# Kernel optimization log

Measured on AMD Instinct MI355X. Metric: run time of the kernel, lower is better.

## Reference

```python
import jax, jax.numpy as jnp
import numpy as np

B, J, HID, INTER, NL = 4096, 16, 128, 64, 4
NEG = -9.0e15
EDGES = [(0,1),(1,2),(2,3),(0,4),(4,5),(5,6),(0,7),(7,8),(8,9),(8,10),(10,11),(11,12),(8,13),(13,14),(14,15)]
GROUPED = [0,7,1,4,2,5,3,6,8,10,9,13,11,14,12,15]  # flattened nodes_group


def _adjacency_nonzeros():
    A = np.zeros((J, J), np.float32)
    for i, j in EDGES:
        A[i, j] = 1.0
        A[j, i] = 1.0
    A += np.eye(J, dtype=np.float32)
    rows, cols = np.nonzero(A)  # row-major, matches torch adj[mask] = e fill order
    return rows.astype(np.int32), cols.astype(np.int32)


def setup_inputs() -> dict:
    key = jax.random.key(0)
    ks = iter(jax.random.split(key, 64))
    rn = lambda shape, s: jax.random.normal(next(ks), shape, jnp.float32) * s
    rows, cols = _adjacency_nonzeros()
    nnz = rows.shape[0]  # 46
    inp = dict(
        x=jax.random.normal(next(ks), (B, J, 2), jnp.float32),
        # input SemGraphConv (2 -> HID) + its BatchNorm
        gc_in_W=rn((2, 2, HID), 0.7), gc_in_e=1.0 + rn((nnz,), 0.3), gc_in_b=rn((HID,), 0.05),
        bn_in_g=1.0 + rn((HID,), 0.05), bn_in_b=rn((HID,), 0.05),
        # 4 residual blocks x 2 graph convs (HID -> HID)
        W_res=rn((2 * NL, 2, HID, HID), 0.08), e_res=1.0 + rn((2 * NL, nnz), 0.3),
        b_res=rn((2 * NL, HID), 0.05),
        bng_res=1.0 + rn((2 * NL, HID), 0.05), bnb_res=rn((2 * NL, HID), 0.05),
        # 5 GraphNonLocal blocks (1 after input + 1 per residual block)
        nl_g_w=rn((NL + 1, INTER, HID), 0.08), nl_g_b=rn((NL + 1, INTER), 0.05),
        nl_t_w=rn((NL + 1, INTER, HID), 0.08), nl_t_b=rn((NL + 1, INTER), 0.05),
        nl_p_w=rn((NL + 1, INTER, HID), 0.08), nl_p_b=rn((NL + 1, INTER), 0.05),
        nl_cp_w=rn((NL + 1, 2 * INTER), 0.08),  # concat_project 1x1 conv, no bias
        nl_W_w=rn((NL + 1, HID, INTER), 0.08), nl_W_b=rn((NL + 1, HID), 0.05),
        nl_bn_g=1.0 + rn((NL + 1, HID), 0.05), nl_bn_b=rn((NL + 1, HID), 0.05),
        # output SemGraphConv (HID -> 3)
        gc_out_W=rn((2, HID, 3), 0.08), gc_out_e=1.0 + rn((nnz,), 0.3), gc_out_b=rn((3,), 0.05),
        # integer constants
        mask_rows=jnp.asarray(rows), mask_cols=jnp.asarray(cols),
        grouped_order=jnp.asarray(GROUPED, jnp.int32),
        restored_order=jnp.asarray(np.argsort(GROUPED), jnp.int32),
    )
    return inp


def reference(x, gc_in_W, gc_in_e, gc_in_b, bn_in_g, bn_in_b,
              W_res, e_res, b_res, bng_res, bnb_res,
              nl_g_w, nl_g_b, nl_t_w, nl_t_b, nl_p_w, nl_p_b,
              nl_cp_w, nl_W_w, nl_W_b, nl_bn_g, nl_bn_b,
              gc_out_W, gc_out_e, gc_out_b,
              mask_rows, mask_cols, grouped_order, restored_order):
    eye = jnp.eye(J, dtype=x.dtype)

    def gconv(h, W, e, b):
        # h: [B, J, F]
        h0 = jnp.einsum('bjf,fo->bjo', h, W[0])
        h1 = jnp.einsum('bjf,fo->bjo', h, W[1])
        logits = jnp.full((J, J), NEG, h.dtype).at[mask_rows, mask_cols].set(e)
        adj = jax.nn.softmax(logits, axis=1)
        diag = jnp.diagonal(adj)                     # adj*I picks diagonal scaling
        off = adj * (1.0 - eye)
        return diag[None, :, None] * h0 + jnp.einsum('ij,bjo->bio', off, h1) + b

    def bn(h, g, bta, axes):
        # training-mode BatchNorm (biased variance), per-channel
        m = h.mean(axes, keepdims=True)
        v = h.var(axes, keepdims=True)
        return (h - m) * jax.lax.rsqrt(v + 1e-5) * g + bta

    def graph_conv(h, W, e, b, gm, gb):
        h = gconv(h, W, e, b)
        h = bn(h, gm[None, None, :], gb[None, None, :], (0, 1))
        return jax.nn.relu(h)

    def nonlocal_block(h, i):
        xo = h[:, grouped_order]          # [B, J, C] regroup joints
        xc = xo.transpose(0, 2, 1)        # [B, C, J]
        conv = lambda w, bb: jnp.einsum('oc,bcj->boj', w, xc) + bb[None, :, None]
        pool = lambda t: t.reshape(B, INTER, J // 2, 2).max(-1)   # MaxPool1d(k=2)
        gx = pool(conv(nl_g_w[i], nl_g_b[i]))                     # [B, I, J/2]
        th = conv(nl_t_w[i], nl_t_b[i])                           # [B, I, J]
        ph = pool(conv(nl_p_w[i], nl_p_b[i]))                     # [B, I, J/2]
        wt, wp = nl_cp_w[i][:INTER], nl_cp_w[i][INTER:]
        # concat_project 1x1 conv over concat(theta,phi) decomposes into a sum
        f = jax.nn.relu(jnp.einsum('bch,c->bh', th, wt)[:, :, None]
                        + jnp.einsum('bcw,c->bw', ph, wp)[:, None, :])  # [B, J, J/2]
        f = f / (J // 2)
        y = jnp.einsum('bhw,bcw->bch', f, gx)                     # [B, I, J]
        Wy = jnp.einsum('oc,bch->boh', nl_W_w[i], y) + nl_W_b[i][None, :, None]
        Wy = bn(Wy, nl_bn_g[i][None, :, None], nl_bn_b[i][None, :, None], (0, 2))
        z = Wy + xc
        return z.transpose(0, 2, 1)[:, restored_order]

    out = graph_conv(x, gc_in_W, gc_in_e, gc_in_b, bn_in_g, bn_in_b)
    out = nonlocal_block(out, 0)
    for i in range(NL):
        res = out
        out = graph_conv(out, W_res[2 * i], e_res[2 * i], b_res[2 * i], bng_res[2 * i], bnb_res[2 * i])
        out = graph_conv(out, W_res[2 * i + 1], e_res[2 * i + 1], b_res[2 * i + 1], bng_res[2 * i + 1], bnb_res[2 * i + 1])
        out = res + out
        out = nonlocal_block(out, i + 1)
    return gconv(out, gc_out_W, gc_out_e, gc_out_b)  # [B, J, 3]
```

## Files before the change

kernel.cpp:

```cpp
#include <hip/hip_runtime.h>

#define B 4096
#define J 16
#define HID 128
#define INTER 64
#define NLAYERS 4
#define NEGV -9000000000000000.0f
#define ELEMS ((size_t)B*16*128)
#define NREP 16
#define SLOT 4096

typedef __attribute__((ext_vector_type(8))) short short8;
typedef __attribute__((ext_vector_type(4))) float f32x4;

static __device__ __forceinline__ unsigned short f2bf(float x) {
    unsigned u = __float_as_uint(x);
    unsigned r = u + 0x7fffu + ((u >> 16) & 1u);
    return (unsigned short)(r >> 16);
}
static __device__ __forceinline__ void splitbf(float x, unsigned short& h, unsigned short& l) {
    h = f2bf(x);
    float hf = __uint_as_float((unsigned)h << 16);
    l = f2bf(x - hf);
}
static __device__ __forceinline__ void splitbf4(float4 v, uint2& hh, uint2& ll) {
    unsigned short h0,l0,h1,l1,h2,l2,h3,l3;
    splitbf(v.x,h0,l0); splitbf(v.y,h1,l1); splitbf(v.z,h2,l2); splitbf(v.w,h3,l3);
    hh = make_uint2((unsigned)h0 | ((unsigned)h1<<16), (unsigned)h2 | ((unsigned)h3<<16));
    ll = make_uint2((unsigned)l0 | ((unsigned)l1<<16), (unsigned)l2 | ((unsigned)l3<<16));
}
static __device__ __forceinline__ f32x4 mfma16(short8 a, short8 b, f32x4 c) {
    return __builtin_amdgcn_mfma_f32_16x16x32_bf16(a, b, c, 0, 0, 0);
}
static __device__ __forceinline__ f32x4 mfma_split(short8 ah, short8 al,
                                                   short8 bh, short8 bl, f32x4 acc) {
    acc = mfma16(ah, bh, acc);
    acc = mfma16(ah, bl, acc);
    acc = mfma16(al, bh, acc);
    return acc;
}
static __device__ __forceinline__ float bfpair(unsigned short h, unsigned short l) {
    return __uint_as_float((unsigned)h << 16) + __uint_as_float((unsigned)l << 16);
}

__global__ void adj_kernel(const float* __restrict__ e_in,
                           const float* __restrict__ e_res,
                           const float* __restrict__ e_out,
                           const int* __restrict__ rows,
                           const int* __restrict__ cols, int nnz,
                           float* __restrict__ off_all,
                           float* __restrict__ diag_all) {
    int m = blockIdx.x;
    int i = threadIdx.x;
    const float* e = (m == 0) ? e_in : (m <= 8) ? e_res + (size_t)(m - 1) * nnz : e_out;
    float l[16];
    for (int j = 0; j < 16; j++) l[j] = NEGV;
    for (int k = 0; k < nnz; k++)
        if (rows[k] == i) l[cols[k]] = e[k];
    float mx = l[0];
    for (int j = 1; j < 16; j++) mx = fmaxf(mx, l[j]);
    float ex[16], s = 0.f;
    for (int j = 0; j < 16; j++) { ex[j] = expf(l[j] - mx); s += ex[j]; }
    float inv = 1.f / s;
    for (int j = 0; j < 16; j++) {
        float a = ex[j] * inv;
        if (j == i) { diag_all[m * 16 + i] = a; a = 0.f; }
        off_all[m * 256 + i * 16 + j] = a;
    }
}

#define WB_N   262144
#define NLW_N  122880
#define NLWW_N 40960
__global__ void prep_w_kernel(const float* __restrict__ W_res,
                              const float* __restrict__ g_w, const float* __restrict__ t_w,
                              const float* __restrict__ p_w, const float* __restrict__ W_w,
                              unsigned short* __restrict__ Wbh, unsigned short* __restrict__ Wbl,
                              unsigned short* __restrict__ nlwh, unsigned short* __restrict__ nlwl,
                              unsigned short* __restrict__ nlWh, unsigned short* __restrict__ nlWl) {
    int i = blockIdx.x * 256 + threadIdx.x;
    unsigned short h, l;
    if (i < WB_N) {
        int lay = i >> 15, rem = i & 32767, n = rem >> 8, k = rem & 255;
        int d = k >> 7, f = k & 127;
        splitbf(W_res[(((lay << 1) | d) * 128 + f) * 128 + n], h, l);
        Wbh[i] = h; Wbl[i] = l;
    } else if (i < WB_N + NLW_N) {
        int j = i - WB_N;
        int lay = j / 24576, r2 = j % 24576;
        int conv = r2 >> 13, oc = r2 & 8191;
        const float* src = conv == 0 ? g_w : conv == 1 ? t_w : p_w;
        splitbf(src[lay * 8192 + oc], h, l);
        nlwh[j] = h; nlwl[j] = l;
    } else if (i < WB_N + NLW_N + NLWW_N) {
        int j = i - WB_N - NLW_N;
        splitbf(W_w[j], h, l);
        nlWh[j] = h; nlWl[j] = l;
    }
}

__global__ void prep_vt_kernel(const float* __restrict__ t_w, const float* __restrict__ t_b,
                               const float* __restrict__ cp_w,
                               float* __restrict__ vt, float* __restrict__ ct) {
    int l = blockIdx.x, c = threadIdx.x;
    float s = 0.f;
    for (int c2 = 0; c2 < 64; c2++)
        s += cp_w[l * 128 + c2] * t_w[(l * 64 + c2) * 128 + c];
    vt[l * 128 + c] = s;
    if (c == 0) {
        float s2 = 0.f;
        for (int c2 = 0; c2 < 64; c2++) s2 += cp_w[l * 128 + c2] * t_b[l * 64 + c2];
        ct[l] = s2;
    }
}

__global__ void finalize_kernel(const float* __restrict__ slot, float* __restrict__ fin) {
    __shared__ float sh[256];
    int t = threadIdx.x;
    float s = 0.f;
    #pragma unroll
    for (int r = 0; r < NREP; r++) s += slot[r * 256 + t];
    sh[t] = s;
    __syncthreads();
    if (t < 128) {
        float m = sh[t] * (1.f / 65536.f);
        float v = sh[128 + t] * (1.f / 65536.f) - m * m;
        fin[t] = m;
        fin[128 + t] = rsqrtf(v + 1e-5f);
    }
}

__global__ __launch_bounds__(256) void gconv_in_kernel(
        const float* __restrict__ x, const float* __restrict__ W,
        const float* __restrict__ bias, const float* __restrict__ off,
        const float* __restrict__ diag, float* __restrict__ out,
        float* __restrict__ stats_out) {
    __shared__ float xs[16][2];
    __shared__ float gs[16][2];
    __shared__ float red[512];
    int b = blockIdx.x, t = threadIdx.x;
    if (t < 32) xs[t >> 1][t & 1] = x[b * 32 + t];
    __syncthreads();
    if (t < 32) {
        int i = t >> 1, f = t & 1;
        float g = 0.f;
        #pragma unroll
        for (int j = 0; j < 16; j++) g += off[i * 16 + j] * xs[j][f];
        gs[i][f] = g;
    }
    __syncthreads();
    int o = t & 127;
    float w00 = W[o], w01 = W[128 + o], w10 = W[256 + o], w11 = W[384 + o], bo = bias[o];
    float s = 0.f, q = 0.f;
    for (int idx = t; idx < 2048; idx += 256) {
        int i = idx >> 7;
        float v = diag[i] * (xs[i][0] * w00 + xs[i][1] * w01)
                + gs[i][0] * w10 + gs[i][1] * w11 + bo;
        out[(size_t)b * 2048 + idx] = v;
        s += v; q += v * v;
    }
    red[t] = s; red[256 + t] = q;
    __syncthreads();
    float* so = stats_out + (b & (NREP - 1)) * 256;
    if (t < 128) {
        atomicAdd(&so[t], red[t] + red[t + 128]);
        atomicAdd(&so[128 + t], red[256 + t] + red[256 + t + 128]);
    }
}

__global__ __launch_bounds__(256) void gconv_mfma_kernel(
        const float* src, const float* wy,
        const float* __restrict__ fin,
        const float* __restrict__ bn_g, const float* __restrict__ bn_b,
        const int* __restrict__ restored, float* zdst,
        const unsigned short* __restrict__ Wbh,
        const unsigned short* __restrict__ Wbl,
        const float* __restrict__ bias,
        const float* __restrict__ off, const float* __restrict__ diag,
        float* dst, float* __restrict__ stats_out) {
    __shared__ float hraw[16][132];
    __shared__ __align__(16) unsigned short ksh[16][264];
    __shared__ __align__(16) unsigned short ksl[16][264];
    __shared__ float offs[256];
    __shared__ float diags[16];
    int t = threadIdx.x;
    offs[t] = off[t];
    if (t < 16) diags[t] = diag[t];
    int c4 = (4 * t) & 127;
    int r0 = t >> 5;
    float4 m4 = make_float4(0,0,0,0), sc4 = make_float4(0,0,0,0), bb4 = make_float4(0,0,0,0);
    if (fin) {
        m4 = *(const float4*)&fin[c4];
        float4 iv = *(const float4*)&fin[128 + c4];
        float4 g4 = *(const float4*)&bn_g[c4];
        bb4 = *(const float4*)&bn_b[c4];
        sc4 = make_float4(iv.x * g4.x, iv.y * g4.y, iv.z * g4.z, iv.w * g4.w);
    }
    int ro0 = 0, ro1 = 0;
    if (wy) { ro0 = restored[r0]; ro1 = restored[r0 + 8]; }
    int b0 = blockIdx.x;
    const float4* src4 = (const float4*)src;
    const float4* wy4  = (const float4*)wy;
    float4 sv0 = src4[(size_t)b0 * 512 + t];
    float4 sv1 = src4[(size_t)b0 * 512 + 256 + t];
    float4 wv0 = make_float4(0,0,0,0), wv1 = make_float4(0,0,0,0);
    if (wy) {
        wv0 = wy4[(size_t)b0 * 512 + ro0 * 32 + (c4 >> 2)];
        wv1 = wy4[(size_t)b0 * 512 + ro1 * 32 + (c4 >> 2)];
    }
    int wv_ = t >> 6, lane = t & 63;
    int mn = lane & 15, kq = (lane >> 4) << 3, qr = (lane >> 4) << 2;

    for (int s = 0; s < 2; s++) {
        int bb_ = blockIdx.x + s * 2048;
        {
            float4 v = sv0;
            if (wy) {
                v.x += (wv0.x - m4.x) * sc4.x + bb4.x;
                v.y += (wv0.y - m4.y) * sc4.y + bb4.y;
                v.z += (wv0.z - m4.z) * sc4.z + bb4.z;
                v.w += (wv0.w - m4.w) * sc4.w + bb4.w;
                ((float4*)zdst)[(size_t)bb_ * 512 + t] = v;
            } else if (fin) {
                v.x = fmaxf((v.x - m4.x) * sc4.x + bb4.x, 0.f);
                v.y = fmaxf((v.y - m4.y) * sc4.y + bb4.y, 0.f);
                v.z = fmaxf((v.z - m4.z) * sc4.z + bb4.z, 0.f);
                v.w = fmaxf((v.w - m4.w) * sc4.w + bb4.w, 0.f);
            }
            *(float4*)&hraw[r0][c4] = v;
            v = sv1;
            if (wy) {
                v.x += (wv1.x - m4.x) * sc4.x + bb4.x;
                v.y += (wv1.y - m4.y) * sc4.y + bb4.y;
                v.z += (wv1.z - m4.z) * sc4.z + bb4.z;
                v.w += (wv1.w - m4.w) * sc4.w + bb4.w;
                ((float4*)zdst)[(size_t)bb_ * 512 + 256 + t] = v;
            } else if (fin) {
                v.x = fmaxf((v.x - m4.x) * sc4.x + bb4.x, 0.f);
                v.y = fmaxf((v.y - m4.y) * sc4.y + bb4.y, 0.f);
                v.z = fmaxf((v.z - m4.z) * sc4.z + bb4.z, 0.f);
                v.w = fmaxf((v.w - m4.w) * sc4.w + bb4.w, 0.f);
            }
            *(float4*)&hraw[r0 + 8][c4] = v;
        }
        if (s == 0) {
            int b1 = blockIdx.x + 2048;
            sv0 = src4[(size_t)b1 * 512 + t];
            sv1 = src4[(size_t)b1 * 512 + 256 + t];
            if (wy) {
                wv0 = wy4[(size_t)b1 * 512 + ro0 * 32 + (c4 >> 2)];
                wv1 = wy4[(size_t)b1 * 512 + ro1 * 32 + (c4 >> 2)];
            }
        }
        __syncthreads();
        for (int u = t; u < 512; u += 256) {
            int i = u >> 5, f4 = (u & 31) << 2;
            float4 hv = *(const float4*)&hraw[i][f4];
            float4 g = make_float4(0.f, 0.f, 0.f, 0.f);
            #pragma unroll
            for (int j = 0; j < 16; j++) {
                float w = offs[i * 16 + j];
                float4 hj = *(const float4*)&hraw[j][f4];
                g.x += w * hj.x; g.y += w * hj.y; g.z += w * hj.z; g.w += w * hj.w;
            }
            float d = diags[i];
            uint2 hh, ll;
            splitbf4(make_float4(d * hv.x, d * hv.y, d * hv.z, d * hv.w), hh, ll);
            *(uint2*)&ksh[i][f4] = hh;
            *(uint2*)&ksl[i][f4] = ll;
            splitbf4(g, hh, ll);
            *(uint2*)&ksh[i][128 + f4] = hh;
            *(uint2*)&ksl[i][128 + f4] = ll;
        }
        __syncthreads();
        int n0 = wv_ << 5;
        f32x4 acc0 = {0.f, 0.f, 0.f, 0.f}, acc1 = {0.f, 0.f, 0.f, 0.f};
        const unsigned short* wh0 = Wbh + (size_t)(n0 + mn) * 256 + kq;
        const unsigned short* wl0 = Wbl + (size_t)(n0 + mn) * 256 + kq;
        #pragma unroll
        for (int k = 0; k < 8; k++) {
            int k0 = k << 5;
            short8 ah = *(const short8*)&ksh[mn][k0 + kq];
            short8 al = *(const short8*)&ksl[mn][k0 + kq];
            acc0 = mfma_split(ah, al, *(const short8*)(wh0 + k0), *(const short8*)(wl0 + k0), acc0);
            acc1 = mfma_split(ah, al, *(const short8*)(wh0 + 4096 + k0), *(const short8*)(wl0 + 4096 + k0), acc1);
        }
        float bias0 = bias[n0 + mn], bias1 = bias[n0 + 16 + mn];
        float s0 = 0.f, q0 = 0.f, s1 = 0.f, q1 = 0.f;
        #pragma unroll
        for (int r = 0; r < 4; r++) {
            int row = qr + r;
            float v0 = acc0[r] + bias0;
            float v1 = acc1[r] + bias1;
            dst[(size_t)bb_ * 2048 + row * 128 + n0 + mn] = v0;
            dst[(size_t)bb_ * 2048 + row * 128 + n0 + 16 + mn] = v1;
            s0 += v0; q0 += v0 * v0; s1 += v1; q1 += v1 * v1;
        }
        s0 += __shfl_xor(s0, 16); s0 += __shfl_xor(s0, 32);
        q0 += __shfl_xor(q0, 16); q0 += __shfl_xor(q0, 32);
        s1 += __shfl_xor(s1, 16); s1 += __shfl_xor(s1, 32);
        q1 += __shfl_xor(q1, 16); q1 += __shfl_xor(q1, 32);
        float* so = stats_out + (bb_ & (NREP - 1)) * 256;
        if (lane < 16) {
            atomicAdd(&so[n0 + mn], s0);
            atomicAdd(&so[128 + n0 + mn], q0);
            atomicAdd(&so[n0 + 16 + mn], s1);
            atomicAdd(&so[128 + n0 + 16 + mn], q1);
        }
        if (s == 0) __syncthreads();
    }
}

#define CG(conv, o, j) cgbuf[((conv) * 64 + (o)) * 17 + (j)]
#define WYL(o, j)      cgbuf[(o) * 17 + (j)]
__global__ __launch_bounds__(512) void nl_a_kernel(
        const float* tsrc, const float* __restrict__ fin,
        const float* __restrict__ bn_g, const float* __restrict__ bn_b,
        const float* res,
        const unsigned short* __restrict__ nlwh,
        const unsigned short* __restrict__ nlwl,
        const float* __restrict__ g_b, const float* __restrict__ p_b,
        const float* __restrict__ cpw,
        const float* __restrict__ vt, const float* __restrict__ ctp,
        const unsigned short* __restrict__ nlWh,
        const unsigned short* __restrict__ nlWl,
        const float* __restrict__ W_b,
        const int* __restrict__ restored,
        float* hdst, float* wydst, float* __restrict__ wst) {
    __shared__ __align__(16) unsigned short xch[16][136];
    __shared__ __align__(16) unsigned short xcl[16][136];
    __shared__ float cgbuf[2176];
    __shared__ float gx[64][9];
    __shared__ float tvp[16][4], pvp[8][8];
    __shared__ float tv[16], pv[8];
    __shared__ float vtl[128];
    __shared__ __align__(16) unsigned short ybh[16][72];
    __shared__ __align__(16) unsigned short ybl[16][72];
    __shared__ float redS[512], redQ[512];
    int b = blockIdx.x, t = threadIdx.x;
    {
        if (t < 128) vtl[t] = vt[t];
        int c4 = (4 * t) & 127;
        int r = t >> 5;
        float4 m4 = *(const float4*)&fin[c4];
        float4 iv = *(const float4*)&fin[128 + c4];
        float4 g4 = *(const float4*)&bn_g[c4];
        float4 bb4 = *(const float4*)&bn_b[c4];
        float4 sc4 = make_float4(iv.x * g4.x, iv.y * g4.y, iv.z * g4.z, iv.w * g4.w);
        float4 v = ((const float4*)tsrc)[(size_t)b * 512 + t];
        v.x = fmaxf((v.x - m4.x) * sc4.x + bb4.x, 0.f);
        v.y = fmaxf((v.y - m4.y) * sc4.y + bb4.y, 0.f);
        v.z = fmaxf((v.z - m4.z) * sc4.z + bb4.z, 0.f);
        v.w = fmaxf((v.w - m4.w) * sc4.w + bb4.w, 0.f);
        if (res) {
            float4 rv = ((const float4*)res)[(size_t)b * 512 + t];
            v.x += rv.x; v.y += rv.y; v.z += rv.z; v.w += rv.w;
        }
        ((float4*)hdst)[(size_t)b * 512 + t] = v;
        int rg = restored[r];
        uint2 hh, ll;
        splitbf4(v, hh, ll);
        *(uint2*)&xch[rg][c4] = hh;
        *(uint2*)&xcl[rg][c4] = ll;
    }
    __syncthreads();
    int w = t >> 6, lane = t & 63;
    int mn = lane & 15, kq = (lane >> 4) << 3, qr = (lane >> 4) << 2;
    {
        int conv = w >> 2;
        int mt = w & 3;
        int wbase = (conv == 0) ? 0 : 128;
        const unsigned short* aph = nlwh + (size_t)(wbase + mt * 16 + mn) * 128 + kq;
        const unsigned short* apl = nlwl + (size_t)(wbase + mt * 16 + mn) * 128 + kq;
        f32x4 acc = {0.f, 0.f, 0.f, 0.f};
        #pragma unroll
        for (int k = 0; k < 4; k++) {
            short8 bh = *(const short8*)&xch[mn][k * 32 + kq];
            short8 bl = *(const short8*)&xcl[mn][k * 32 + kq];
            acc = mfma_split(*(const short8*)(aph + k * 32), *(const short8*)(apl + k * 32),
                             bh, bl, acc);
        }
        const float* bias = (conv == 0) ? g_b : p_b;
        #pragma unroll
        for (int r = 0; r < 4; r++) {
            int o = mt * 16 + qr + r;
            CG(conv, o, mn) = acc[r] + bias[o];
        }
    }
    __syncthreads();
    {
        int c = t >> 3, w2 = t & 7;
        gx[c][w2] = fmaxf(CG(0, c, 2 * w2), CG(0, c, 2 * w2 + 1));
        if (t < 64) {
            int w2b = t & 7, ch = t >> 3;
            float ss = 0.f;
            for (int cc = ch * 8; cc < ch * 8 + 8; cc++)
                ss += fmaxf(CG(1, cc, 2 * w2b), CG(1, cc, 2 * w2b + 1)) * cpw[64 + cc];
            pvp[w2b][ch] = ss;
        } else if (t < 128) {
            int u = t - 64, j = u & 15, ch = u >> 4;
            float ss = 0.f;
            int c0 = ch * 32;
            for (int cc = c0; cc < c0 + 32; cc += 2) {
                unsigned hh = *(const unsigned*)&xch[j][cc];
                unsigned ll = *(const unsigned*)&xcl[j][cc];
                float v0 = bfpair((unsigned short)hh, (unsigned short)ll);
                float v1 = bfpair((unsigned short)(hh >> 16), (unsigned short)(ll >> 16));
                ss += vtl[cc] * v0 + vtl[cc + 1] * v1;
            }
            tvp[j][ch] = ss;
        }
    }
    __syncthreads();
    if (t < 16) {
        tv[t] = tvp[t][0] + tvp[t][1] + tvp[t][2] + tvp[t][3] + ctp[0];
    } else if (t < 24) {
        int w2 = t - 16;
        float ss = 0.f;
        #pragma unroll
        for (int ch = 0; ch < 8; ch++) ss += pvp[w2][ch];
        pv[w2] = ss;
    }
    __syncthreads();
    #pragma unroll
    for (int u2 = 0; u2 < 2; u2++) {
        int u = t + u2 * 512;
        int j = u >> 6, c = u & 63;
        float ss = 0.f;
        #pragma unroll
        for (int w2 = 0; w2 < 8; w2++)
            ss += fmaxf(tv[j] + pv[w2], 0.f) * gx[c][w2];
        unsigned short h, l;
        splitbf(ss * 0.125f, h, l);
        ybh[j][c] = h; ybl[j][c] = l;
    }
    __syncthreads();
    {
        int mt = w;
        short8 byh0 = *(const short8*)&ybh[mn][kq];
        short8 byh1 = *(const short8*)&ybh[mn][32 + kq];
        short8 byl0 = *(const short8*)&ybl[mn][kq];
        short8 byl1 = *(const short8*)&ybl[mn][32 + kq];
        const unsigned short* aph = nlWh + (size_t)(mt * 16 + mn) * 64 + kq;
        const unsigned short* apl = nlWl + (size_t)(mt * 16 + mn) * 64 + kq;
        f32x4 acc = {0.f, 0.f, 0.f, 0.f};
        acc = mfma_split(*(const short8*)aph, *(const short8*)apl, byh0, byl0, acc);
        acc = mfma_split(*(const short8*)(aph + 32), *(const short8*)(apl + 32), byh1, byl1, acc);
        #pragma unroll
        for (int r = 0; r < 4; r++) {
            int o = mt * 16 + qr + r;
            WYL(o, mn) = acc[r] + W_b[o];
        }
    }
    __syncthreads();
    {
        int c = t & 127;
        float ss = 0.f, qq = 0.f;
        #pragma unroll
        for (int u2 = 0; u2 < 4; u2++) {
            int idx = t + u2 * 512;
            int j = idx >> 7;
            float v = WYL(c, j);
            wydst[(size_t)b * 2048 + idx] = v;
            ss += v; qq += v * v;
        }
        redS[t] = ss; redQ[t] = qq;
        __syncthreads();
        float* so = wst + (b & (NREP - 1)) * 256;
        if (t < 128) {
            float s4 = redS[t] + redS[t + 128] + redS[t + 256] + redS[t + 384];
            float q4 = redQ[t] + redQ[t + 128] + redQ[t + 256] + redQ[t + 384];
            atomicAdd(&so[t], s4);
            atomicAdd(&so[128 + t], q4);
        }
    }
}

__global__ __launch_bounds__(256) void gconv_out_kernel(
        const float* __restrict__ h, const float* __restrict__ wy,
        const float* __restrict__ fin,
        const float* __restrict__ nlg, const float* __restrict__ nlb,
        const int* __restrict__ restored,
        const float* __restrict__ W,
        const float* __restrict__ bias, const float* __restrict__ off,
        const float* __restrict__ diag, float* __restrict__ out) {
    __shared__ float hs[16][132];
    __shared__ float gsv[16][132];
    __shared__ float offs[256];
    __shared__ float p0[48][4], p1[48][4];
    int b = blockIdx.x, t = threadIdx.x;
    offs[t] = off[t];
    {
        int c = t & 127;
        float mean = fin[c];
        float inv = fin[128 + c] * nlg[c];
        float bb = nlb[c];
        for (int idx = t; idx < 2048; idx += 256) {
            int r = idx >> 7;
            float wval = wy[(size_t)b * 2048 + restored[r] * 128 + c];
            hs[r][c] = (wval - mean) * inv + bb + h[(size_t)b * 2048 + idx];
        }
    }
    __syncthreads();
    for (int idx = t; idx < 2048; idx += 256) {
        int i = idx >> 7, f = idx & 127;
        float g = 0.f;
        #pragma unroll
        for (int j = 0; j < 16; j++) g += offs[i * 16 + j] * hs[j][f];
        gsv[i][f] = g;
    }
    __syncthreads();
    if (t < 192) {
        int oid = t >> 2, chunk = t & 3;
        int i = oid / 3, o = oid % 3;
        float a0 = 0.f, a1 = 0.f;
        int f0 = chunk * 32;
        for (int f = f0; f < f0 + 32; f++) {
            a0 += hs[i][f] * W[f * 3 + o];
            a1 += gsv[i][f] * W[384 + f * 3 + o];
        }
        p0[oid][chunk] = a0; p1[oid][chunk] = a1;
    }
    __syncthreads();
    if (t < 48) {
        int i = t / 3, o = t % 3;
        float a0 = p0[t][0] + p0[t][1] + p0[t][2] + p0[t][3];
        float a1 = p1[t][0] + p1[t][1] + p1[t][2] + p1[t][3];
        out[(size_t)b * 48 + t] = diag[i] * a0 + a1 + bias[o];
    }
}

extern "C" void kernel_launch(void* const* d_in, const int* in_sizes, int n_in,
                              void* d_out, int out_size, void* d_ws, size_t ws_size,
                              hipStream_t stream) {
    (void)n_in; (void)out_size; (void)ws_size;
    const float* x        = (const float*)d_in[0];
    const float* gc_in_W  = (const float*)d_in[1];
    const float* gc_in_e  = (const float*)d_in[2];
    const float* gc_in_b  = (const float*)d_in[3];
    const float* bn_in_g  = (const float*)d_in[4];
    const float* bn_in_b  = (const float*)d_in[5];
    const float* W_res    = (const float*)d_in[6];
    const float* e_res    = (const float*)d_in[7];
    const float* b_res    = (const float*)d_in[8];
    const float* bng_res  = (const float*)d_in[9];
    const float* bnb_res  = (const float*)d_in[10];
    const float* nl_g_w   = (const float*)d_in[11];
    const float* nl_g_b   = (const float*)d_in[12];
    const float* nl_t_w   = (const float*)d_in[13];
    const float* nl_t_b   = (const float*)d_in[14];
    const float* nl_p_w   = (const float*)d_in[15];
    const float* nl_p_b   = (const float*)d_in[16];
    const float* nl_cp_w  = (const float*)d_in[17];
    const float* nl_W_w   = (const float*)d_in[18];
    const float* nl_W_b   = (const float*)d_in[19];
    const float* nl_bn_g  = (const float*)d_in[20];
    const float* nl_bn_b  = (const float*)d_in[21];
    const float* gc_out_W = (const float*)d_in[22];
    const float* gc_out_e = (const float*)d_in[23];
    const float* gc_out_b = (const float*)d_in[24];
    const int*   mask_rows = (const int*)d_in[25];
    const int*   mask_cols = (const int*)d_in[26];
    const int*   restored  = (const int*)d_in[28];
    int nnz = in_sizes[2];

    float* ws       = (float*)d_ws;
    float* off_all  = ws;
    float* diag_all = ws + 2560;
    float* stats    = ws + 2720;
    float* fin      = ws + 60064;
    float* vt       = ws + 63664;
    float* ct       = ws + 64304;
    unsigned short* Wbh  = (unsigned short*)(ws + 65536);
    unsigned short* Wbl  = Wbh + WB_N;
    unsigned short* nlwh = Wbl + WB_N;
    unsigned short* nlwl = nlwh + NLW_N;
    unsigned short* nlWh = nlwl + NLW_N;
    unsigned short* nlWl = nlWh + NLWW_N;
    float* Z = ws + 491520;
    float* T = Z + ELEMS;

    hipMemsetAsync(stats, 0, 14 * SLOT * sizeof(float), stream);
    adj_kernel<<<10, 16, 0, stream>>>(gc_in_e, e_res, gc_out_e, mask_rows, mask_cols,
                                      nnz, off_all, diag_all);
    prep_w_kernel<<<(WB_N + NLW_N + NLWW_N + 255) / 256, 256, 0, stream>>>(
        W_res, nl_g_w, nl_t_w, nl_p_w, nl_W_w, Wbh, Wbl, nlwh, nlwl, nlWh, nlWl);
    prep_vt_kernel<<<5, 128, 0, stream>>>(nl_t_w, nl_t_b, nl_cp_w, vt, ct);

    gconv_in_kernel<<<B, 256, 0, stream>>>(x, gc_in_W, gc_in_b, off_all, diag_all,
                                           T, stats);
    finalize_kernel<<<1, 256, 0, stream>>>(stats, fin);
    nl_a_kernel<<<B, 512, 0, stream>>>(T, fin, bn_in_g, bn_in_b, nullptr,
                                       nlwh, nlwl, nl_g_b, nl_p_b, nl_cp_w,
                                       vt, ct, nlWh, nlWl, nl_W_b, restored,
                                       Z, T, stats + SLOT);
    finalize_kernel<<<1, 256, 0, stream>>>(stats + SLOT, fin + 256);

    int sl = 1;
    for (int i = 0; i < NLAYERS; i++) {
        int l0 = 2 * i, l1 = 2 * i + 1, li = i + 1;
        gconv_mfma_kernel<<<2048, 256, 0, stream>>>(
            Z, T, fin + (size_t)sl * 256,
            nl_bn_g + i * 128, nl_bn_b + i * 128, restored, Z,
            Wbh + (size_t)l0 * 32768, Wbl + (size_t)l0 * 32768, b_res + l0 * 128,
            off_all + (1 + l0) * 256, diag_all + (1 + l0) * 16, T,
            stats + (size_t)(sl + 1) * SLOT);
        finalize_kernel<<<1, 256, 0, stream>>>(stats + (size_t)(sl + 1) * SLOT,
                                               fin + (size_t)(sl + 1) * 256);
        gconv_mfma_kernel<<<2048, 256, 0, stream>>>(
            T, nullptr, fin + (size_t)(sl + 1) * 256,
            bng_res + l0 * 128, bnb_res + l0 * 128, nullptr, nullptr,
            Wbh + (size_t)l1 * 32768, Wbl + (size_t)l1 * 32768, b_res + l1 * 128,
            off_all + (1 + l1) * 256, diag_all + (1 + l1) * 16, T,
            stats + (size_t)(sl + 2) * SLOT);
        finalize_kernel<<<1, 256, 0, stream>>>(stats + (size_t)(sl + 2) * SLOT,
                                               fin + (size_t)(sl + 2) * 256);
        nl_a_kernel<<<B, 512, 0, stream>>>(
            T, fin + (size_t)(sl + 2) * 256,
            bng_res + l1 * 128, bnb_res + l1 * 128, Z,
            nlwh + li * 24576, nlwl + li * 24576,
            nl_g_b + li * 64, nl_p_b + li * 64, nl_cp_w + li * 128,
            vt + li * 128, ct + li, nlWh + li * 8192, nlWl + li * 8192,
            nl_W_b + li * 128, restored, Z, T,
            stats + (size_t)(sl + 3) * SLOT);
        finalize_kernel<<<1, 256, 0, stream>>>(stats + (size_t)(sl + 3) * SLOT,
                                               fin + (size_t)(sl + 3) * 256);
        sl += 3;
    }
    gconv_out_kernel<<<B, 256, 0, stream>>>(Z, T, fin + (size_t)sl * 256,
                                            nl_bn_g + NLAYERS * 128, nl_bn_b + NLAYERS * 128,
                                            restored, gc_out_W, gc_out_b,
                                            off_all + 9 * 256, diag_all + 9 * 16,
                                            (float*)d_out);
}
```

Measured before the change: 899.1 us.

## Fuse BN stats finalize into consumer kernels and process two samples per nl block

Removes the 13 single-block finalize launches. Each consumer kernel now sums the NREP partial stat slots itself and computes mean and inverse std in shared memory. The nonlocal kernel is also restructured to handle two batch samples per block with the next sample's loads prefetched, halving its grid. The shuffle-based reductions for tv/pv replace two extra shared-memory passes and one barrier. In exchange, every block redundantly re-reads and reduces the stat slots, and the non-local kernel has fewer blocks in flight.

```diff
diff --git a/kernel.cpp b/kernel.cpp
--- a/kernel.cpp
+++ b/kernel.cpp
@@ -114,22 +114,6 @@
     }
 }
 
-__global__ void finalize_kernel(const float* __restrict__ slot, float* __restrict__ fin) {
-    __shared__ float sh[256];
-    int t = threadIdx.x;
-    float s = 0.f;
-    #pragma unroll
-    for (int r = 0; r < NREP; r++) s += slot[r * 256 + t];
-    sh[t] = s;
-    __syncthreads();
-    if (t < 128) {
-        float m = sh[t] * (1.f / 65536.f);
-        float v = sh[128 + t] * (1.f / 65536.f) - m * m;
-        fin[t] = m;
-        fin[128 + t] = rsqrtf(v + 1e-5f);
-    }
-}
-
 __global__ __launch_bounds__(256) void gconv_in_kernel(
         const float* __restrict__ x, const float* __restrict__ W,
         const float* __restrict__ bias, const float* __restrict__ off,
@@ -170,7 +154,7 @@
 
 __global__ __launch_bounds__(256) void gconv_mfma_kernel(
         const float* src, const float* wy,
-        const float* __restrict__ fin,
+        const float* __restrict__ stats_in,
         const float* __restrict__ bn_g, const float* __restrict__ bn_b,
         const int* __restrict__ restored, float* zdst,
         const unsigned short* __restrict__ Wbh,
@@ -186,16 +170,15 @@
     int t = threadIdx.x;
     offs[t] = off[t];
     if (t < 16) diags[t] = diag[t];
+    float* hrawf = &hraw[0][0];
+    {
+        float ssum = 0.f;
+        #pragma unroll
+        for (int rr = 0; rr < NREP; rr++) ssum += stats_in[rr * 256 + t];
+        hrawf[t] = ssum;
+    }
     int c4 = (4 * t) & 127;
     int r0 = t >> 5;
-    float4 m4 = make_float4(0,0,0,0), sc4 = make_float4(0,0,0,0), bb4 = make_float4(0,0,0,0);
-    if (fin) {
-        m4 = *(const float4*)&fin[c4];
-        float4 iv = *(const float4*)&fin[128 + c4];
-        float4 g4 = *(const float4*)&bn_g[c4];
-        bb4 = *(const float4*)&bn_b[c4];
-        sc4 = make_float4(iv.x * g4.x, iv.y * g4.y, iv.z * g4.z, iv.w * g4.w);
-    }
     int ro0 = 0, ro1 = 0;
     if (wy) { ro0 = restored[r0]; ro1 = restored[r0 + 8]; }
     int b0 = blockIdx.x;
@@ -208,6 +191,22 @@
         wv0 = wy4[(size_t)b0 * 512 + ro0 * 32 + (c4 >> 2)];
         wv1 = wy4[(size_t)b0 * 512 + ro1 * 32 + (c4 >> 2)];
     }
+    __syncthreads();
+    float4 m4, sc4, bb4;
+    {
+        const float K = 1.f / 65536.f;
+        float4 g4 = *(const float4*)&bn_g[c4];
+        bb4 = *(const float4*)&bn_b[c4];
+        float m0 = hrawf[c4]     * K, m1 = hrawf[c4 + 1] * K;
+        float m2 = hrawf[c4 + 2] * K, m3 = hrawf[c4 + 3] * K;
+        float i0 = rsqrtf(hrawf[128 + c4]     * K - m0 * m0 + 1e-5f);
+        float i1 = rsqrtf(hrawf[128 + c4 + 1] * K - m1 * m1 + 1e-5f);
+        float i2 = rsqrtf(hrawf[128 + c4 + 2] * K - m2 * m2 + 1e-5f);
+        float i3 = rsqrtf(hrawf[128 + c4 + 3] * K - m3 * m3 + 1e-5f);
+        m4 = make_float4(m0, m1, m2, m3);
+        sc4 = make_float4(i0 * g4.x, i1 * g4.y, i2 * g4.z, i3 * g4.w);
+    }
+    __syncthreads();
     int wv_ = t >> 6, lane = t & 63;
     int mn = lane & 15, kq = (lane >> 4) << 3, qr = (lane >> 4) << 2;
 
@@ -221,7 +220,7 @@
                 v.z += (wv0.z - m4.z) * sc4.z + bb4.z;
                 v.w += (wv0.w - m4.w) * sc4.w + bb4.w;
                 ((float4*)zdst)[(size_t)bb_ * 512 + t] = v;
-            } else if (fin) {
+            } else {
                 v.x = fmaxf((v.x - m4.x) * sc4.x + bb4.x, 0.f);
                 v.y = fmaxf((v.y - m4.y) * sc4.y + bb4.y, 0.f);
                 v.z = fmaxf((v.z - m4.z) * sc4.z + bb4.z, 0.f);
@@ -235,7 +234,7 @@
                 v.z += (wv1.z - m4.z) * sc4.z + bb4.z;
                 v.w += (wv1.w - m4.w) * sc4.w + bb4.w;
                 ((float4*)zdst)[(size_t)bb_ * 512 + 256 + t] = v;
-            } else if (fin) {
+            } else {
                 v.x = fmaxf((v.x - m4.x) * sc4.x + bb4.x, 0.f);
                 v.y = fmaxf((v.y - m4.y) * sc4.y + bb4.y, 0.f);
                 v.z = fmaxf((v.z - m4.z) * sc4.z + bb4.z, 0.f);
@@ -314,7 +313,7 @@
 #define CG(conv, o, j) cgbuf[((conv) * 64 + (o)) * 17 + (j)]
 #define WYL(o, j)      cgbuf[(o) * 17 + (j)]
 __global__ __launch_bounds__(512) void nl_a_kernel(
-        const float* tsrc, const float* __restrict__ fin,
+        const float* tsrc, const float* __restrict__ stats_in,
         const float* __restrict__ bn_g, const float* __restrict__ bn_b,
         const float* res,
         const unsigned short* __restrict__ nlwh,
@@ -331,154 +330,175 @@
     __shared__ __align__(16) unsigned short xcl[16][136];
     __shared__ float cgbuf[2176];
     __shared__ float gx[64][9];
-    __shared__ float tvp[16][4], pvp[8][8];
     __shared__ float tv[16], pv[8];
     __shared__ float vtl[128];
     __shared__ __align__(16) unsigned short ybh[16][72];
     __shared__ __align__(16) unsigned short ybl[16][72];
     __shared__ float redS[512], redQ[512];
-    int b = blockIdx.x, t = threadIdx.x;
+    int t = threadIdx.x;
+    int b0 = blockIdx.x;
+    const float4* tsrc4 = (const float4*)tsrc;
+    const float4* res4  = (const float4*)res;
+    float4 sv = tsrc4[(size_t)b0 * 512 + t];
+    float4 rv = make_float4(0.f, 0.f, 0.f, 0.f);
+    if (res) rv = res4[(size_t)b0 * 512 + t];
+    if (t < 256) {
+        float ssum = 0.f;
+        #pragma unroll
+        for (int rr = 0; rr < NREP; rr++) ssum += stats_in[rr * 256 + t];
+        redS[t] = ssum;
+    }
+    if (t < 128) vtl[t] = vt[t];
+    int c4 = (4 * t) & 127;
+    int r0 = t >> 5;
+    int rg = restored[r0];
+    __syncthreads();
+    float4 m4, sc4, bb4;
     {
-        if (t < 128) vtl[t] = vt[t];
-        int c4 = (4 * t) & 127;
-        int r = t >> 5;
-        float4 m4 = *(const float4*)&fin[c4];
-        float4 iv = *(const float4*)&fin[128 + c4];
+        const float K = 1.f / 65536.f;
         float4 g4 = *(const float4*)&bn_g[c4];
-        float4 bb4 = *(const float4*)&bn_b[c4];
-        float4 sc4 = make_float4(iv.x * g4.x, iv.y * g4.y, iv.z * g4.z, iv.w * g4.w);
-        float4 v = ((const float4*)tsrc)[(size_t)b * 512 + t];
-        v.x = fmaxf((v.x - m4.x) * sc4.x + bb4.x, 0.f);
-        v.y = fmaxf((v.y - m4.y) * sc4.y + bb4.y, 0.f);
-        v.z = fmaxf((v.z - m4.z) * sc4.z + bb4.z, 0.f);
-        v.w = fmaxf((v.w - m4.w) * sc4.w + bb4.w, 0.f);
-        if (res) {
-            float4 rv = ((const float4*)res)[(size_t)b * 512 + t];
-            v.x += rv.x; v.y += rv.y; v.z += rv.z; v.w += rv.w;
-        }
-        ((float4*)hdst)[(size_t)b * 512 + t] = v;
-        int rg = restored[r];
-        uint2 hh, ll;
-        splitbf4(v, hh, ll);
-        *(uint2*)&xch[rg][c4] = hh;
-        *(uint2*)&xcl[rg][c4] = ll;
-    }
-    __syncthreads();
+        bb4 = *(const float4*)&bn_b[c4];
+        float m0 = redS[c4]     * K, m1 = redS[c4 + 1] * K;
+        float m2 = redS[c4 + 2] * K, m3 = redS[c4 + 3] * K;
+        float i0 = rsqrtf(redS[128 + c4]     * K - m0 * m0 + 1e-5f);
+        float i1 = rsqrtf(redS[128 + c4 + 1] * K - m1 * m1 + 1e-5f);
+        float i2 = rsqrtf(redS[128 + c4 + 2] * K - m2 * m2 + 1e-5f);
+        float i3 = rsqrtf(redS[128 + c4 + 3] * K - m3 * m3 + 1e-5f);
+        m4 = make_float4(m0, m1, m2, m3);
+        sc4 = make_float4(i0 * g4.x, i1 * g4.y, i2 * g4.z, i3 * g4.w);
+    }
     int w = t >> 6, lane = t & 63;
     int mn = lane & 15, kq = (lane >> 4) << 3, qr = (lane >> 4) << 2;
-    {
-        int conv = w >> 2;
-        int mt = w & 3;
-        int wbase = (conv == 0) ? 0 : 128;
-        const unsigned short* aph = nlwh + (size_t)(wbase + mt * 16 + mn) * 128 + kq;
-        const unsigned short* apl = nlwl + (size_t)(wbase + mt * 16 + mn) * 128 + kq;
-        f32x4 acc = {0.f, 0.f, 0.f, 0.f};
-        #pragma unroll
-        for (int k = 0; k < 4; k++) {
-            short8 bh = *(const short8*)&xch[mn][k * 32 + kq];
-            short8 bl = *(const short8*)&xcl[mn][k * 32 + kq];
-            acc = mfma_split(*(const short8*)(aph + k * 32), *(const short8*)(apl + k * 32),
-                             bh, bl, acc);
-        }
-        const float* bias = (conv == 0) ? g_b : p_b;
-        #pragma unroll
-        for (int r = 0; r < 4; r++) {
-            int o = mt * 16 + qr + r;
-            CG(conv, o, mn) = acc[r] + bias[o];
-        }
-    }
-    __syncthreads();
-    {
-        int c = t >> 3, w2 = t & 7;
-        gx[c][w2] = fmaxf(CG(0, c, 2 * w2), CG(0, c, 2 * w2 + 1));
-        if (t < 64) {
-            int w2b = t & 7, ch = t >> 3;
+
+    for (int s = 0; s < 2; s++) {
+        int bb = b0 + s * 2048;
+        {
+            float4 v = sv;
+            v.x = fmaxf((v.x - m4.x) * sc4.x + bb4.x, 0.f);
+            v.y = fmaxf((v.y - m4.y) * sc4.y + bb4.y, 0.f);
+            v.z = fmaxf((v.z - m4.z) * sc4.z + bb4.z, 0.f);
+            v.w = fmaxf((v.w - m4.w) * sc4.w + bb4.w, 0.f);
+            if (res) { v.x += rv.x; v.y += rv.y; v.z += rv.z; v.w += rv.w; }
+            ((float4*)hdst)[(size_t)bb * 512 + t] = v;
+            uint2 hh, ll;
+            splitbf4(v, hh, ll);
+            *(uint2*)&xch[rg][c4] = hh;
+            *(uint2*)&xcl[rg][c4] = ll;
+        }
+        if (s == 0) {
+            sv = tsrc4[(size_t)(b0 + 2048) * 512 + t];
+            if (res) rv = res4[(size_t)(b0 + 2048) * 512 + t];
+        }
+        __syncthreads();
+        {
+            int conv = w >> 2;
+            int mt = w & 3;
+            int wbase = (conv == 0) ? 0 : 128;
+            const unsigned short* aph = nlwh + (size_t)(wbase + mt * 16 + mn) * 128 + kq;
+            const unsigned short* apl = nlwl + (size_t)(wbase + mt * 16 + mn) * 128 + kq;
+            f32x4 acc = {0.f, 0.f, 0.f, 0.f};
+            #pragma unroll
+            for (int k = 0; k < 4; k++) {
+                short8 bh = *(const short8*)&xch[mn][k * 32 + kq];
+                short8 bl = *(const short8*)&xcl[mn][k * 32 + kq];
+                acc = mfma_split(*(const short8*)(aph + k * 32), *(const short8*)(apl + k * 32),
+                                 bh, bl, acc);
+            }
+            const float* biasp = (conv == 0) ? g_b : p_b;
+            #pragma unroll
+            for (int r = 0; r < 4; r++) {
+                int o = mt * 16 + qr + r;
+                CG(conv, o, mn) = acc[r] + biasp[o];
+            }
+        }
+        __syncthreads();
+        {
+            int c = t >> 3, w2 = t & 7;
+            gx[c][w2] = fmaxf(CG(0, c, 2 * w2), CG(0, c, 2 * w2 + 1));
+            if (t < 64) {
+                int ch = t >> 3;
+                float ss = 0.f;
+                for (int cc = ch * 8; cc < ch * 8 + 8; cc++)
+                    ss += fmaxf(CG(1, cc, 2 * w2), CG(1, cc, 2 * w2 + 1)) * cpw[64 + cc];
+                ss += __shfl_xor(ss, 8);
+                ss += __shfl_xor(ss, 16);
+                ss += __shfl_xor(ss, 32);
+                if (t < 8) pv[t] = ss;
+            } else if (t < 128) {
+                int u = t - 64, j = u & 15, ch = u >> 4;
+                float ss = 0.f;
+                int c0 = ch * 32;
+                for (int cc = c0; cc < c0 + 32; cc += 2) {
+                    unsigned hh = *(const unsigned*)&xch[j][cc];
+                    unsigned ll = *(const unsigned*)&xcl[j][cc];
+                    float v0 = bfpair((unsigned short)hh, (unsigned short)ll);
+                    float v1 = bfpair((unsigned short)(hh >> 16), (unsigned short)(ll >> 16));
+                    ss += vtl[cc] * v0 + vtl[cc + 1] * v1;
+                }
+                ss += __shfl_xor(ss, 16);
+                ss += __shfl_xor(ss, 32);
+                if (u < 16) tv[u] = ss + ctp[0];
+            }
+        }
+        __syncthreads();
+        #pragma unroll
+        for (int u2 = 0; u2 < 2; u2++) {
+            int u = t + u2 * 512;
+            int j = u >> 6, c = u & 63;
             float ss = 0.f;
-            for (int cc = ch * 8; cc < ch * 8 + 8; cc++)
-                ss += fmaxf(CG(1, cc, 2 * w2b), CG(1, cc, 2 * w2b + 1)) * cpw[64 + cc];
-            pvp[w2b][ch] = ss;
-        } else if (t < 128) {
-            int u = t - 64, j = u & 15, ch = u >> 4;
-            float ss = 0.f;
-            int c0 = ch * 32;
-            for (int cc = c0; cc < c0 + 32; cc += 2) {
-                unsigned hh = *(const unsigned*)&xch[j][cc];
-                unsigned ll = *(const unsigned*)&xcl[j][cc];
-                float v0 = bfpair((unsigned short)hh, (unsigned short)ll);
-                float v1 = bfpair((unsigned short)(hh >> 16), (unsigned short)(ll >> 16));
-                ss += vtl[cc] * v0 + vtl[cc + 1] * v1;
-            }
-            tvp[j][ch] = ss;
-        }
-    }
-    __syncthreads();
-    if (t < 16) {
-        tv[t] = tvp[t][0] + tvp[t][1] + tvp[t][2] + tvp[t][3] + ctp[0];
-    } else if (t < 24) {
-        int w2 = t - 16;
-        float ss = 0.f;
-        #pragma unroll
-        for (int ch = 0; ch < 8; ch++) ss += pvp[w2][ch];
-        pv[w2] = ss;
-    }
-    __syncthreads();
-    #pragma unroll
-    for (int u2 = 0; u2 < 2; u2++) {
-        int u = t + u2 * 512;
-        int j = u >> 6, c = u & 63;
-        float ss = 0.f;
-        #pragma unroll
-        for (int w2 = 0; w2 < 8; w2++)
-            ss += fmaxf(tv[j] + pv[w2], 0.f) * gx[c][w2];
-        unsigned short h, l;
-        splitbf(ss * 0.125f, h, l);
-        ybh[j][c] = h; ybl[j][c] = l;
-    }
-    __syncthreads();
-    {
-        int mt = w;
-        short8 byh0 = *(const short8*)&ybh[mn][kq];
-        short8 byh1 = *(const short8*)&ybh[mn][32 + kq];
-        short8 byl0 = *(const short8*)&ybl[mn][kq];
-        short8 byl1 = *(const short8*)&ybl[mn][32 + kq];
-        const unsigned short* aph = nlWh + (size_t)(mt * 16 + mn) * 64 + kq;
-        const unsigned short* apl = nlWl + (size_t)(mt * 16 + mn) * 64 + kq;
-        f32x4 acc = {0.f, 0.f, 0.f, 0.f};
-        acc = mfma_split(*(const short8*)aph, *(const short8*)apl, byh0, byl0, acc);
-        acc = mfma_split(*(const short8*)(aph + 32), *(const short8*)(apl + 32), byh1, byl1, acc);
-        #pragma unroll
-        for (int r = 0; r < 4; r++) {
-            int o = mt * 16 + qr + r;
-            WYL(o, mn) = acc[r] + W_b[o];
-        }
-    }
-    __syncthreads();
-    {
-        int c = t & 127;
-        float ss = 0.f, qq = 0.f;
-        #pragma unroll
-        for (int u2 = 0; u2 < 4; u2++) {
-            int idx = t + u2 * 512;
-            int j = idx >> 7;
-            float v = WYL(c, j);
-            wydst[(size_t)b * 2048 + idx] = v;
-            ss += v; qq += v * v;
-        }
-        redS[t] = ss; redQ[t] = qq;
+            #pragma unroll
+            for (int w2 = 0; w2 < 8; w2++)
+                ss += fmaxf(tv[j] + pv[w2], 0.f) * gx[c][w2];
+            unsigned short h2, l2;
+            splitbf(ss * 0.125f, h2, l2);
+            ybh[j][c] = h2; ybl[j][c] = l2;
+        }
         __syncthreads();
-        float* so = wst + (b & (NREP - 1)) * 256;
-        if (t < 128) {
-            float s4 = redS[t] + redS[t + 128] + redS[t + 256] + redS[t + 384];
-            float q4 = redQ[t] + redQ[t + 128] + redQ[t + 256] + redQ[t + 384];
-            atomicAdd(&so[t], s4);
-            atomicAdd(&so[128 + t], q4);
+        {
+            int mt = w;
+            short8 byh0 = *(const short8*)&ybh[mn][kq];
+            short8 byh1 = *(const short8*)&ybh[mn][32 + kq];
+            short8 byl0 = *(const short8*)&ybl[mn][kq];
+            short8 byl1 = *(const short8*)&ybl[mn][32 + kq];
+            const unsigned short* aph = nlWh + (size_t)(mt * 16 + mn) * 64 + kq;
+            const unsigned short* apl = nlWl + (size_t)(mt * 16 + mn) * 64 + kq;
+            f32x4 acc = {0.f, 0.f, 0.f, 0.f};
+            acc = mfma_split(*(const short8*)aph, *(const short8*)apl, byh0, byl0, acc);
+            acc = mfma_split(*(const short8*)(aph + 32), *(const short8*)(apl + 32), byh1, byl1, acc);
+            #pragma unroll
+            for (int r = 0; r < 4; r++) {
+                int o = mt * 16 + qr + r;
+                WYL(o, mn) = acc[r] + W_b[o];
+            }
+        }
+        __syncthreads();
+        {
+            int c = t & 127;
+            float ss = 0.f, qq = 0.f;
+            #pragma unroll
+            for (int u2 = 0; u2 < 4; u2++) {
+                int idx = t + u2 * 512;
+                int j = idx >> 7;
+                float v = WYL(c, j);
+                wydst[(size_t)bb * 2048 + idx] = v;
+                ss += v; qq += v * v;
+            }
+            redS[t] = ss; redQ[t] = qq;
+            __syncthreads();
+            float* so = wst + (bb & (NREP - 1)) * 256;
+            if (t < 128) {
+                float s4 = redS[t] + redS[t + 128] + redS[t + 256] + redS[t + 384];
+                float q4 = redQ[t] + redQ[t + 128] + redQ[t + 256] + redQ[t + 384];
+                atomicAdd(&so[t], s4);
+                atomicAdd(&so[128 + t], q4);
+            }
         }
     }
 }
 
 __global__ __launch_bounds__(256) void gconv_out_kernel(
         const float* __restrict__ h, const float* __restrict__ wy,
-        const float* __restrict__ fin,
+        const float* __restrict__ stats_in,
         const float* __restrict__ nlg, const float* __restrict__ nlb,
         const int* __restrict__ restored,
         const float* __restrict__ W,
@@ -490,15 +510,29 @@
     __shared__ float p0[48][4], p1[48][4];
     int b = blockIdx.x, t = threadIdx.x;
     offs[t] = off[t];
+    float* hsf = &hs[0][0];
     {
-        int c = t & 127;
-        float mean = fin[c];
-        float inv = fin[128 + c] * nlg[c];
-        float bb = nlb[c];
+        float ssum = 0.f;
+        #pragma unroll
+        for (int rr = 0; rr < NREP; rr++) ssum += stats_in[rr * 256 + t];
+        hsf[t] = ssum;
+    }
+    __syncthreads();
+    int c = t & 127;
+    float mean, inv, bbv;
+    {
+        const float K = 1.f / 65536.f;
+        mean = hsf[c] * K;
+        float varv = hsf[128 + c] * K - mean * mean;
+        inv = rsqrtf(varv + 1e-5f) * nlg[c];
+        bbv = nlb[c];
+    }
+    __syncthreads();
+    {
         for (int idx = t; idx < 2048; idx += 256) {
             int r = idx >> 7;
             float wval = wy[(size_t)b * 2048 + restored[r] * 128 + c];
-            hs[r][c] = (wval - mean) * inv + bb + h[(size_t)b * 2048 + idx];
+            hs[r][c] = (wval - mean) * inv + bbv + h[(size_t)b * 2048 + idx];
         }
     }
     __syncthreads();
@@ -568,7 +602,6 @@
     float* off_all  = ws;
     float* diag_all = ws + 2560;
     float* stats    = ws + 2720;
-    float* fin      = ws + 60064;
     float* vt       = ws + 63664;
     float* ct       = ws + 64304;
     unsigned short* Wbh  = (unsigned short*)(ws + 65536);
@@ -589,45 +622,37 @@
 
     gconv_in_kernel<<<B, 256, 0, stream>>>(x, gc_in_W, gc_in_b, off_all, diag_all,
                                            T, stats);
-    finalize_kernel<<<1, 256, 0, stream>>>(stats, fin);
-    nl_a_kernel<<<B, 512, 0, stream>>>(T, fin, bn_in_g, bn_in_b, nullptr,
-                                       nlwh, nlwl, nl_g_b, nl_p_b, nl_cp_w,
-                                       vt, ct, nlWh, nlWl, nl_W_b, restored,
-                                       Z, T, stats + SLOT);
-    finalize_kernel<<<1, 256, 0, stream>>>(stats + SLOT, fin + 256);
+    nl_a_kernel<<<B / 2, 512, 0, stream>>>(T, stats, bn_in_g, bn_in_b, nullptr,
+                                           nlwh, nlwl, nl_g_b, nl_p_b, nl_cp_w,
+                                           vt, ct, nlWh, nlWl, nl_W_b, restored,
+                                           Z, T, stats + SLOT);
 
     int sl = 1;
     for (int i = 0; i < NLAYERS; i++) {
         int l0 = 2 * i, l1 = 2 * i + 1, li = i + 1;
         gconv_mfma_kernel<<<2048, 256, 0, stream>>>(
-            Z, T, fin + (size_t)sl * 256,
+            Z, T, stats + (size_t)sl * SLOT,
             nl_bn_g + i * 128, nl_bn_b + i * 128, restored, Z,
             Wbh + (size_t)l0 * 32768, Wbl + (size_t)l0 * 32768, b_res + l0 * 128,
             off_all + (1 + l0) * 256, diag_all + (1 + l0) * 16, T,
             stats + (size_t)(sl + 1) * SLOT);
-        finalize_kernel<<<1, 256, 0, stream>>>(stats + (size_t)(sl + 1) * SLOT,
-                                               fin + (size_t)(sl + 1) * 256);
         gconv_mfma_kernel<<<2048, 256, 0, stream>>>(
-            T, nullptr, fin + (size_t)(sl + 1) * 256,
+            T, nullptr, stats + (size_t)(sl + 1) * SLOT,
             bng_res + l0 * 128, bnb_res + l0 * 128, nullptr, nullptr,
             Wbh + (size_t)l1 * 32768, Wbl + (size_t)l1 * 32768, b_res + l1 * 128,
             off_all + (1 + l1) * 256, diag_all + (1 + l1) * 16, T,
             stats + (size_t)(sl + 2) * SLOT);
-        finalize_kernel<<<1, 256, 0, stream>>>(stats + (size_t)(sl + 2) * SLOT,
-                                               fin + (size_t)(sl + 2) * 256);
-        nl_a_kernel<<<B, 512, 0, stream>>>(
-            T, fin + (size_t)(sl + 2) * 256,
+        nl_a_kernel<<<B / 2, 512, 0, stream>>>(
+            T, stats + (size_t)(sl + 2) * SLOT,
             bng_res + l1 * 128, bnb_res + l1 * 128, Z,
             nlwh + li * 24576, nlwl + li * 24576,
             nl_g_b + li * 64, nl_p_b + li * 64, nl_cp_w + li * 128,
             vt + li * 128, ct + li, nlWh + li * 8192, nlWl + li * 8192,
             nl_W_b + li * 128, restored, Z, T,
             stats + (size_t)(sl + 3) * SLOT);
-        finalize_kernel<<<1, 256, 0, stream>>>(stats + (size_t)(sl + 3) * SLOT,
-                                               fin + (size_t)(sl + 3) * 256);
         sl += 3;
     }
-    gconv_out_kernel<<<B, 256, 0, stream>>>(Z, T, fin + (size_t)sl * 256,
+    gconv_out_kernel<<<B, 256, 0, stream>>>(Z, T, stats + (size_t)sl * SLOT,
                                             nl_bn_g + NLAYERS * 128, nl_bn_b + NLAYERS * 128,
                                             restored, gc_out_W, gc_out_b,
                                             off_all + 9 * 256, diag_all + 9 * 16,
```

After: 926.2 us. 1.03x slower.
